# Kernel optimization log

Hardware: AMD Instinct MI355X
Metric: run time of the kernel (lower is better)

## Reference

```python
import jax, jax.numpy as jnp
import numpy as np

TOP_K = 2
LN_EPS = 1e-5
GATE_EPS = 1e-6


def setup_inputs() -> dict:
    key = jax.random.key(0)
    ks = jax.random.split(key, 5)
    B, D, E, H, O = 16384, 1200, 8, 1024, 1
    x = jax.random.normal(ks[0], (B, D), dtype=jnp.float32)
    w_gate = jax.random.normal(ks[1], (D, E), dtype=jnp.float32) * 0.05
    W1 = jax.random.normal(ks[2], (E, D, H), dtype=jnp.float32) * (1.0 / np.sqrt(D))
    b1 = jnp.zeros((E, H), dtype=jnp.float32)
    g1 = jnp.ones((E, H), dtype=jnp.float32)   # LayerNorm weight
    be1 = jnp.zeros((E, H), dtype=jnp.float32)  # LayerNorm bias
    W2 = jax.random.normal(ks[3], (E, H, O), dtype=jnp.float32) * (1.0 / np.sqrt(H))
    b2 = jnp.zeros((E, O), dtype=jnp.float32)
    return {"x": x, "w_gate": w_gate, "W1": W1, "b1": b1, "g1": g1, "be1": be1, "W2": W2, "b2": b2}


def reference(x, w_gate, W1, b1, g1, be1, W2, b2):
    B = x.shape[0]
    # --- top-k gating (eval mode: no noise) ---
    probs = jax.nn.softmax(x @ w_gate, axis=1)                 # [B, E]
    top_vals, top_idx = jax.lax.top_k(probs, TOP_K)            # [B, k]
    top_gates = top_vals / (jnp.sum(top_vals, axis=1, keepdims=True) + GATE_EPS)
    gates = jnp.zeros_like(probs).at[jnp.arange(B)[:, None], top_idx].set(top_gates)  # [B, E]
    # --- per-expert MLP (computed densely for all experts; gates zero out non-selected) ---
    h = jnp.einsum('bd,edh->beh', x, W1) + b1                  # [B, E, H]
    mu = jnp.mean(h, axis=-1, keepdims=True)
    var = jnp.var(h, axis=-1, keepdims=True)
    h = (h - mu) * jax.lax.rsqrt(var + LN_EPS) * g1 + be1      # LayerNorm
    h = jax.nn.relu(h)
    out = jax.nn.sigmoid(jnp.einsum('beh,eho->beo', h, W2) + b2)  # [B, E, O]
    # --- scatter/combine: weighted sum over experts ---
    y = jnp.einsum('be,beo->bo', gates, out)                   # [B, O]
    return y
```

## Files before the change

kernel.cpp:

```cpp
#include <hip/hip_runtime.h>
#include <hip/hip_bf16.h>
#include <stdint.h>

#define B_ROWS 16384
#define D_IN   1200
#define D_PAD  1216
#define N_EXP  8
#define H_DIM  1024
#define CAP    33792
#define N_TILES 264
#define LN_EPS 1e-5f
#define GATE_EPS 1e-6f
#define CNT_STRIDE 16

#define O_CNT    0
#define O_POFF   512
#define O_CNT2   576
#define O_TOPI   1088
#define O_TOPG   132160
#define O_PROWC  263232
#define O_PGATEC 398400
#define O_XBF    533568
#define O_W1T    40381888
#define O_HBUF   60304832

#define GATING_BLOCKS (B_ROWS / 32)
#define W1T_BLOCKS    (19 * 16 * 8)

typedef short bf16x8 __attribute__((ext_vector_type(8)));
typedef short short8 __attribute__((ext_vector_type(8)));
typedef short short4v __attribute__((ext_vector_type(4)));
typedef float f32x4 __attribute__((ext_vector_type(4)));

__device__ __forceinline__ void load_lds16(const void* gptr, void* ldsptr) {
    __builtin_amdgcn_global_load_lds(
        (__attribute__((address_space(1))) void*)const_cast<void*>(gptr),
        (__attribute__((address_space(3))) void*)ldsptr, 16, 0, 0);
}

__device__ __forceinline__ short4v pack_bf16x4(float4 a) {
    union { short4v v; __hip_bfloat16 h[4]; } u;
    u.h[0] = __float2bfloat16(a.x); u.h[1] = __float2bfloat16(a.y);
    u.h[2] = __float2bfloat16(a.z); u.h[3] = __float2bfloat16(a.w);
    return u.v;
}

__global__ __launch_bounds__(256) void gating_w1t_kernel(
    const float* __restrict__ x, const float* __restrict__ wg,
    const float* __restrict__ W1,
    int* __restrict__ topIdx, float* __restrict__ topGate,
    __hip_bfloat16* __restrict__ w1t, __hip_bfloat16* __restrict__ xbf)
{
    __shared__ float tile[2][32][33];
    int bx = blockIdx.x;
    int tid = threadIdx.x;

    if (bx < GATING_BLOCKS) {
        int widx = tid >> 6;
        int lane = tid & 63;
        int rowbase = bx * 32 + widx * 8;
        const float* xw = x + (long)rowbase * D_IN;

        float acc[8][8];
#pragma unroll
        for (int r = 0; r < 8; ++r)
#pragma unroll
            for (int e = 0; e < N_EXP; ++e) acc[r][e] = 0.f;

        for (int i = lane; i < 304; i += 64) {
            if (i < 300) {
                const float4* wv4 = (const float4*)(wg + (long)i * 32);
                float4 w0 = wv4[0], w1v = wv4[1], w2 = wv4[2], w3 = wv4[3],
                       w4 = wv4[4], w5 = wv4[5], w6 = wv4[6], w7 = wv4[7];
#pragma unroll
                for (int r = 0; r < 8; ++r) {
                    float4 xv = ((const float4*)(xw + (long)r * D_IN))[i];
                    acc[r][0] += xv.x * w0.x + xv.y * w2.x + xv.z * w4.x + xv.w * w6.x;
                    acc[r][1] += xv.x * w0.y + xv.y * w2.y + xv.z * w4.y + xv.w * w6.y;
                    acc[r][2] += xv.x * w0.z + xv.y * w2.z + xv.z * w4.z + xv.w * w6.z;
                    acc[r][3] += xv.x * w0.w + xv.y * w2.w + xv.z * w4.w + xv.w * w6.w;
                    acc[r][4] += xv.x * w1v.x + xv.y * w3.x + xv.z * w5.x + xv.w * w7.x;
                    acc[r][5] += xv.x * w1v.y + xv.y * w3.y + xv.z * w5.y + xv.w * w7.y;
                    acc[r][6] += xv.x * w1v.z + xv.y * w3.z + xv.z * w5.z + xv.w * w7.z;
                    acc[r][7] += xv.x * w1v.w + xv.y * w3.w + xv.z * w5.w + xv.w * w7.w;
                    ((short4v*)(xbf + (long)(rowbase + r) * D_PAD))[i] = pack_bf16x4(xv);
                }
            } else {
#pragma unroll
                for (int r = 0; r < 8; ++r)
                    ((short4v*)(xbf + (long)(rowbase + r) * D_PAD))[i] = (short4v){0, 0, 0, 0};
            }
        }

#pragma unroll
        for (int r = 0; r < 8; ++r)
#pragma unroll
            for (int e = 0; e < N_EXP; ++e) {
                float v = acc[r][e];
#pragma unroll
                for (int off = 32; off > 0; off >>= 1) v += __shfl_xor(v, off, 64);
                acc[r][e] = v;
            }

        float my[N_EXP];
#pragma unroll
        for (int e = 0; e < N_EXP; ++e) my[e] = acc[0][e];
#pragma unroll
        for (int r = 1; r < 8; ++r)
#pragma unroll
            for (int e = 0; e < N_EXP; ++e)
                if (lane == r) my[e] = acc[r][e];

        if (lane < 8) {
            float m = my[0];
#pragma unroll
            for (int e = 1; e < N_EXP; ++e) m = fmaxf(m, my[e]);
            float p[N_EXP], s = 0.f;
#pragma unroll
            for (int e = 0; e < N_EXP; ++e) { p[e] = expf(my[e] - m); s += p[e]; }
            int i0 = 0;
#pragma unroll
            for (int e = 1; e < N_EXP; ++e) if (p[e] > p[i0]) i0 = e;
            int i1 = (i0 == 0) ? 1 : 0;
#pragma unroll
            for (int e = 0; e < N_EXP; ++e) if (e != i0 && p[e] > p[i1]) i1 = e;
            float v0 = p[i0] / s, v1 = p[i1] / s;
            float inv = 1.f / (v0 + v1 + GATE_EPS);
            int row = rowbase + lane;
            ((int2*)topIdx)[row] = make_int2(i0, i1);
            ((float2*)topGate)[row] = make_float2(v0 * inv, v1 * inv);
        }
    } else if (bx == GATING_BLOCKS) {
        short8* xrow = (short8*)(xbf + (long)B_ROWS * D_PAD);
        if (tid < 152) xrow[tid] = (short8){0, 0, 0, 0, 0, 0, 0, 0};
    } else {
        int b = bx - GATING_BLOCKS - 1;
        int d0 = (b % 19) * 64;
        int h0 = ((b / 19) % 16) * 64;
        int e = b / (19 * 16);
        const float* src = W1 + (long)e * D_IN * H_DIM;

        int hseg = tid & 7;
        int hs = tid & 15;
        int dr = tid >> 4;
        (void)hseg;
#pragma unroll
        for (int s = 0; s < 4; ++s) {
            int dl = dr + 16 * s;
            int d = d0 + dl;
            float4 v = (d < D_IN)
                ? ((const float4*)(src + (long)d * H_DIM + h0))[hs]
                : (float4){0.f, 0.f, 0.f, 0.f};
            int T = dl >> 5, drl = dl & 31;
            int hl = hs * 4;
            int Th = hl >> 5;
            int hh = hl & 31;
            (void)T; (void)hh;
            tile[Th][drl][hh + 0] = v.x;
            tile[Th][drl][hh + 1] = v.y;
            tile[Th][drl][hh + 2] = v.z;
            tile[Th][drl][hh + 3] = v.w;
            if (s == 1) {
                __syncthreads();
                int r2 = tid;
                int T2 = r2 >> 7, rr = r2 & 127;
                int hl2 = rr >> 2, dseg = rr & 3;
                float f[8];
#pragma unroll
                for (int j = 0; j < 8; ++j) f[j] = tile[T2][dseg * 8 + j][hl2];
                union { short8 v8; __hip_bfloat16 hh8[8]; } u;
#pragma unroll
                for (int j = 0; j < 8; ++j) u.hh8[j] = __float2bfloat16(f[j]);
                int h = h0 + T2 * 32 + hl2;
                ((short8*)(w1t + (long)e * H_DIM * D_PAD + (long)h * D_PAD + d0))[dseg] = u.v8;
                __syncthreads();
            }
        }
        __syncthreads();
        {
            int T2 = tid >> 7, rr = tid & 127;
            int hl2 = rr >> 2, dseg = rr & 3;
            float f[8];
#pragma unroll
            for (int j = 0; j < 8; ++j) f[j] = tile[T2][dseg * 8 + j][hl2];
            union { short8 v8; __hip_bfloat16 hh8[8]; } u;
#pragma unroll
            for (int j = 0; j < 8; ++j) u.hh8[j] = __float2bfloat16(f[j]);
            int h = h0 + T2 * 32 + hl2;
            ((short8*)(w1t + (long)e * H_DIM * D_PAD + (long)h * D_PAD + d0 + 32))[dseg] = u.v8;
        }
    }
}

__global__ __launch_bounds__(256) void hist_kernel(
    const int* __restrict__ topIdx, int* __restrict__ cnt, float* __restrict__ y)
{
    __shared__ int lcnt[N_EXP];
    int tid = threadIdx.x;
    if (tid < N_EXP) lcnt[tid] = 0;
    __syncthreads();
    int row = blockIdx.x * 256 + tid;
    y[row] = 0.f;
    int2 e = ((const int2*)topIdx)[row];
    atomicAdd(&lcnt[e.x], 1);
    atomicAdd(&lcnt[e.y], 1);
    __syncthreads();
    if (tid < N_EXP) atomicAdd(&cnt[tid * CNT_STRIDE], lcnt[tid]);
}

__global__ void offsets_kernel(const int* __restrict__ cnt, int* __restrict__ poff)
{
    if (threadIdx.x == 0 && blockIdx.x == 0) {
        int o = 0;
        for (int e = 0; e < N_EXP; ++e) {
            poff[e] = o;
            o += (cnt[e * CNT_STRIDE] + 127) & ~127;
        }
        poff[N_EXP] = o;
    }
}

__global__ __launch_bounds__(256) void scatter_kernel(
    const int* __restrict__ topIdx, const float* __restrict__ topGate,
    const int* __restrict__ cnt, const int* __restrict__ poff, int* __restrict__ cnt2,
    int* __restrict__ pairRowC, float* __restrict__ pairGateC)
{
    int tid = threadIdx.x;
    int b = blockIdx.x;

    {
        int p = b * 256 + tid;
        int e = 0;
        while (e < N_EXP - 1 && p >= poff[e + 1]) ++e;
        if (p - poff[e] >= cnt[e * CNT_STRIDE]) {
            pairRowC[p] = B_ROWS;
            pairGateC[p] = 0.f;
        }
    }
    if (b >= B_ROWS / 256) return;

    __shared__ int lcnt[N_EXP];
    __shared__ int base[N_EXP];
    if (tid < N_EXP) lcnt[tid] = 0;
    __syncthreads();
    int row = b * 256 + tid;
    int2 e = ((const int2*)topIdx)[row];
    float2 g = ((const float2*)topGate)[row];
    int s0 = atomicAdd(&lcnt[e.x], 1);
    int s1 = atomicAdd(&lcnt[e.y], 1);
    __syncthreads();
    if (tid < N_EXP) base[tid] = atomicAdd(&cnt2[tid * CNT_STRIDE], lcnt[tid]);
    __syncthreads();
    int p0 = poff[e.x] + base[e.x] + s0;
    pairRowC[p0] = row; pairGateC[p0] = g.x;
    int p1 = poff[e.y] + base[e.y] + s1;
    pairRowC[p1] = row; pairGateC[p1] = g.y;
}

__global__ __launch_bounds__(256) void gemm_kernel(
    const __hip_bfloat16* __restrict__ xbf, const __hip_bfloat16* __restrict__ w1t,
    const float* __restrict__ b1, const int* __restrict__ poff,
    const int* __restrict__ pairRowC,
    __hip_bfloat16* __restrict__ hbuf)
{
    int bi = blockIdx.x;
    int xcd = bi & 7;
    int j = bi >> 3;
    int col0 = (j & 7) << 7;
    int rt = xcd * 33 + (j >> 3);
    int row0 = rt << 7;
    if (row0 >= poff[N_EXP]) return;
    int e = 0;
    while (e < N_EXP - 1 && row0 >= poff[e + 1]) ++e;

    __shared__ short lA[128 * 32];
    __shared__ short lB[128 * 32];

    int t = threadIdx.x;
    int lane = t & 63, w = t >> 6;
    int wm = (w >> 1) * 64, wn = (w & 1) * 64;
    int l15 = lane & 15, quad = lane >> 4;
    int qsw = quad ^ ((l15 >> 1) & 3);

    f32x4 acc[4][4];
#pragma unroll
    for (int i = 0; i < 4; ++i)
#pragma unroll
        for (int j2 = 0; j2 < 4; ++j2) acc[i][j2] = (f32x4){0.f, 0.f, 0.f, 0.f};

    int r1 = t >> 2, seg = t & 3;
    int sw = seg ^ ((r1 >> 1) & 3);
    int ridx1 = pairRowC[row0 + r1];
    int ridx2 = pairRowC[row0 + 64 + r1];
    const __hip_bfloat16* Arow1 = xbf + (long)ridx1 * D_PAD + sw * 8;
    const __hip_bfloat16* Arow2 = xbf + (long)ridx2 * D_PAD + sw * 8;
    const __hip_bfloat16* Bb = w1t + (long)e * H_DIM * D_PAD + (long)col0 * D_PAD;
    const __hip_bfloat16* Brow1 = Bb + (long)r1 * D_PAD + sw * 8;
    const __hip_bfloat16* Brow2 = Bb + (long)(r1 + 64) * D_PAD + sw * 8;
    char* lAc = (char*)lA;
    char* lBc = (char*)lB;

    for (int kt = 0; kt < D_PAD / 32; ++kt) {
        __syncthreads();
        int k0 = kt * 32;
        load_lds16(Arow1 + k0, lAc + t * 16);
        load_lds16(Arow2 + k0, lAc + t * 16 + 4096);
        load_lds16(Brow1 + k0, lBc + t * 16);
        load_lds16(Brow2 + k0, lBc + t * 16 + 4096);
        __syncthreads();

        bf16x8 af[4], bfr[4];
#pragma unroll
        for (int i = 0; i < 4; ++i)
            af[i] = *(const bf16x8*)(lAc + (wm + i * 16 + l15) * 64 + qsw * 16);
#pragma unroll
        for (int j2 = 0; j2 < 4; ++j2)
            bfr[j2] = *(const bf16x8*)(lBc + (wn + j2 * 16 + l15) * 64 + qsw * 16);
#pragma unroll
        for (int i = 0; i < 4; ++i)
#pragma unroll
            for (int j2 = 0; j2 < 4; ++j2)
                acc[i][j2] = __builtin_amdgcn_mfma_f32_16x16x32_bf16(af[i], bfr[j2], acc[i][j2], 0, 0, 0);
    }

#pragma unroll
    for (int i = 0; i < 4; ++i) {
        int lr = wm + i * 16 + quad * 4;
#pragma unroll
        for (int j2 = 0; j2 < 4; ++j2) {
            int gc = col0 + wn + j2 * 16 + l15;
            float bias = b1[e * H_DIM + gc];
#pragma unroll
            for (int r = 0; r < 4; ++r) {
                float v = acc[i][j2][r] + bias;
                hbuf[(long)(row0 + lr + r) * H_DIM + gc] = __float2bfloat16(v);
            }
        }
    }
}

__global__ __launch_bounds__(256) void ln_head_kernel(
    const __hip_bfloat16* __restrict__ hbuf, const int* __restrict__ cnt, const int* __restrict__ poff,
    const int* __restrict__ pairRowC, const float* __restrict__ pairGateC,
    const float* __restrict__ g1, const float* __restrict__ be1,
    const float* __restrict__ W2, const float* __restrict__ b2,
    float* __restrict__ y)
{
    int p = blockIdx.x;
    if (p >= poff[N_EXP]) return;
    int e = 0;
    while (e < N_EXP - 1 && p >= poff[e + 1]) ++e;
    if (p - poff[e] >= cnt[e * CNT_STRIDE]) return;

    int row = pairRowC[p];
    float gate = pairGateC[p];
    int tid = threadIdx.x;
    int w = tid >> 6;
    const __hip_bfloat16* hr = hbuf + (long)p * H_DIM;

    union { short4v s; __hip_bfloat16 h[4]; } hv;
    hv.s = ((const short4v*)hr)[tid];
    float v[4];
    float sum = 0.f, sumsq = 0.f;
#pragma unroll
    for (int k = 0; k < 4; ++k) {
        v[k] = __bfloat162float(hv.h[k]);
        sum += v[k];
        sumsq += v[k] * v[k];
    }
#pragma unroll
    for (int off = 32; off > 0; off >>= 1) {
        sum += __shfl_down(sum, off);
        sumsq += __shfl_down(sumsq, off);
    }
    __shared__ float rs[4], rq[4];
    if ((tid & 63) == 0) { rs[w] = sum; rq[w] = sumsq; }
    __syncthreads();
    float tot = rs[0] + rs[1] + rs[2] + rs[3];
    float totq = rq[0] + rq[1] + rq[2] + rq[3];
    float mu = tot * (1.f / H_DIM);
    float var = totq * (1.f / H_DIM) - mu * mu;
    float rstd = rsqrtf(var + LN_EPS);

    float4 gv = ((const float4*)(g1 + e * H_DIM))[tid];
    float4 bv = ((const float4*)(be1 + e * H_DIM))[tid];
    float4 wv = ((const float4*)(W2 + e * H_DIM))[tid];
    float z;
    {
        float hn0 = fmaxf((v[0] - mu) * rstd * gv.x + bv.x, 0.f);
        float hn1 = fmaxf((v[1] - mu) * rstd * gv.y + bv.y, 0.f);
        float hn2 = fmaxf((v[2] - mu) * rstd * gv.z + bv.z, 0.f);
        float hn3 = fmaxf((v[3] - mu) * rstd * gv.w + bv.w, 0.f);
        z = hn0 * wv.x + hn1 * wv.y + hn2 * wv.z + hn3 * wv.w;
    }
#pragma unroll
    for (int off = 32; off > 0; off >>= 1) z += __shfl_down(z, off);
    __syncthreads();
    if ((tid & 63) == 0) rs[w] = z;
    __syncthreads();
    if (tid == 0) {
        float zt = rs[0] + rs[1] + rs[2] + rs[3] + b2[e];
        float o = 1.f / (1.f + expf(-zt));
        atomicAdd(&y[row], gate * o);
    }
}

extern "C" void kernel_launch(void* const* d_in, const int* in_sizes, int n_in,
                              void* d_out, int out_size, void* d_ws, size_t ws_size,
                              hipStream_t stream)
{
    const float* x   = (const float*)d_in[0];
    const float* wg  = (const float*)d_in[1];
    const float* W1  = (const float*)d_in[2];
    const float* b1  = (const float*)d_in[3];
    const float* g1  = (const float*)d_in[4];
    const float* be1 = (const float*)d_in[5];
    const float* W2  = (const float*)d_in[6];
    const float* b2  = (const float*)d_in[7];
    float* y = (float*)d_out;

    char* ws = (char*)d_ws;
    int*   cnt       = (int*)(ws + O_CNT);
    int*   poff      = (int*)(ws + O_POFF);
    int*   cnt2      = (int*)(ws + O_CNT2);
    int*   topIdx    = (int*)(ws + O_TOPI);
    float* topGate   = (float*)(ws + O_TOPG);
    int*   pairRowC  = (int*)(ws + O_PROWC);
    float* pairGateC = (float*)(ws + O_PGATEC);
    __hip_bfloat16* xbf  = (__hip_bfloat16*)(ws + O_XBF);
    __hip_bfloat16* w1t  = (__hip_bfloat16*)(ws + O_W1T);
    __hip_bfloat16* hbuf = (__hip_bfloat16*)(ws + O_HBUF);

    hipMemsetAsync(ws, 0, 1088, stream);

    gating_w1t_kernel<<<GATING_BLOCKS + 1 + W1T_BLOCKS, 256, 0, stream>>>(
        x, wg, W1, topIdx, topGate, w1t, xbf);
    hist_kernel<<<B_ROWS / 256, 256, 0, stream>>>(topIdx, cnt, y);
    offsets_kernel<<<1, 64, 0, stream>>>(cnt, poff);
    scatter_kernel<<<CAP / 256, 256, 0, stream>>>(topIdx, topGate, cnt, poff, cnt2,
                                                  pairRowC, pairGateC);
    gemm_kernel<<<N_TILES * 8, 256, 0, stream>>>(xbf, w1t, b1, poff, pairRowC, hbuf);
    ln_head_kernel<<<CAP, 256, 0, stream>>>(hbuf, cnt, poff, pairRowC, pairGateC,
                                            g1, be1, W2, b2, y);
}
```

Measured before the change: 312.8 us.

## Fuse histogram into gating, deepen GEMM K-step, one wave per row in LN head

Expert counting moves into the gating blocks through an LDS histogram, which removes a separate kernel launch; the zeroing of y moves into the scatter kernel. The GEMM main loop now stages two 32-wide K slices per iteration, halving the number of barrier pairs at the cost of doubled LDS usage. The LayerNorm/head kernel assigns one wavefront per pair row, with four rows per block, so reductions use only shuffles and no block barriers. It also launches a quarter as many blocks.

New measurement: 315.3 us. About the same (+0.8%).

```diff
diff --git a/kernel.cpp b/kernel.cpp
--- a/kernel.cpp
+++ b/kernel.cpp
@@ -49,13 +49,18 @@
     const float* __restrict__ x, const float* __restrict__ wg,
     const float* __restrict__ W1,
     int* __restrict__ topIdx, float* __restrict__ topGate,
+    int* __restrict__ cnt,
     __hip_bfloat16* __restrict__ w1t, __hip_bfloat16* __restrict__ xbf)
 {
     __shared__ float tile[2][32][33];
+    __shared__ int lhist[N_EXP];
     int bx = blockIdx.x;
     int tid = threadIdx.x;
 
     if (bx < GATING_BLOCKS) {
+        if (tid < N_EXP) lhist[tid] = 0;
+        __syncthreads();
+
         int widx = tid >> 6;
         int lane = tid & 63;
         int rowbase = bx * 32 + widx * 8;
@@ -129,7 +134,11 @@
             int row = rowbase + lane;
             ((int2*)topIdx)[row] = make_int2(i0, i1);
             ((float2*)topGate)[row] = make_float2(v0 * inv, v1 * inv);
-        }
+            atomicAdd(&lhist[i0], 1);
+            atomicAdd(&lhist[i1], 1);
+        }
+        __syncthreads();
+        if (tid < N_EXP) atomicAdd(&cnt[tid * CNT_STRIDE], lhist[tid]);
     } else if (bx == GATING_BLOCKS) {
         short8* xrow = (short8*)(xbf + (long)B_ROWS * D_PAD);
         if (tid < 152) xrow[tid] = (short8){0, 0, 0, 0, 0, 0, 0, 0};
@@ -140,10 +149,8 @@
         int e = b / (19 * 16);
         const float* src = W1 + (long)e * D_IN * H_DIM;
 
-        int hseg = tid & 7;
         int hs = tid & 15;
         int dr = tid >> 4;
-        (void)hseg;
 #pragma unroll
         for (int s = 0; s < 4; ++s) {
             int dl = dr + 16 * s;
@@ -151,19 +158,17 @@
             float4 v = (d < D_IN)
                 ? ((const float4*)(src + (long)d * H_DIM + h0))[hs]
                 : (float4){0.f, 0.f, 0.f, 0.f};
-            int T = dl >> 5, drl = dl & 31;
+            int drl = dl & 31;
             int hl = hs * 4;
             int Th = hl >> 5;
             int hh = hl & 31;
-            (void)T; (void)hh;
             tile[Th][drl][hh + 0] = v.x;
             tile[Th][drl][hh + 1] = v.y;
             tile[Th][drl][hh + 2] = v.z;
             tile[Th][drl][hh + 3] = v.w;
             if (s == 1) {
                 __syncthreads();
-                int r2 = tid;
-                int T2 = r2 >> 7, rr = r2 & 127;
+                int T2 = tid >> 7, rr = tid & 127;
                 int hl2 = rr >> 2, dseg = rr & 3;
                 float f[8];
 #pragma unroll
@@ -192,22 +197,6 @@
     }
 }
 
-__global__ __launch_bounds__(256) void hist_kernel(
-    const int* __restrict__ topIdx, int* __restrict__ cnt, float* __restrict__ y)
-{
-    __shared__ int lcnt[N_EXP];
-    int tid = threadIdx.x;
-    if (tid < N_EXP) lcnt[tid] = 0;
-    __syncthreads();
-    int row = blockIdx.x * 256 + tid;
-    y[row] = 0.f;
-    int2 e = ((const int2*)topIdx)[row];
-    atomicAdd(&lcnt[e.x], 1);
-    atomicAdd(&lcnt[e.y], 1);
-    __syncthreads();
-    if (tid < N_EXP) atomicAdd(&cnt[tid * CNT_STRIDE], lcnt[tid]);
-}
-
 __global__ void offsets_kernel(const int* __restrict__ cnt, int* __restrict__ poff)
 {
     if (threadIdx.x == 0 && blockIdx.x == 0) {
@@ -223,7 +212,7 @@
 __global__ __launch_bounds__(256) void scatter_kernel(
     const int* __restrict__ topIdx, const float* __restrict__ topGate,
     const int* __restrict__ cnt, const int* __restrict__ poff, int* __restrict__ cnt2,
-    int* __restrict__ pairRowC, float* __restrict__ pairGateC)
+    int* __restrict__ pairRowC, float* __restrict__ pairGateC, float* __restrict__ y)
 {
     int tid = threadIdx.x;
     int b = blockIdx.x;
@@ -239,11 +228,13 @@
     }
     if (b >= B_ROWS / 256) return;
 
+    int row = b * 256 + tid;
+    y[row] = 0.f;
+
     __shared__ int lcnt[N_EXP];
     __shared__ int base[N_EXP];
     if (tid < N_EXP) lcnt[tid] = 0;
     __syncthreads();
-    int row = b * 256 + tid;
     int2 e = ((const int2*)topIdx)[row];
     float2 g = ((const float2*)topGate)[row];
     int s0 = atomicAdd(&lcnt[e.x], 1);
@@ -273,8 +264,8 @@
     int e = 0;
     while (e < N_EXP - 1 && row0 >= poff[e + 1]) ++e;
 
-    __shared__ short lA[128 * 32];
-    __shared__ short lB[128 * 32];
+    __shared__ short lA[2][128 * 32];
+    __shared__ short lB[2][128 * 32];
 
     int t = threadIdx.x;
     int lane = t & 63, w = t >> 6;
@@ -297,30 +288,37 @@
     const __hip_bfloat16* Bb = w1t + (long)e * H_DIM * D_PAD + (long)col0 * D_PAD;
     const __hip_bfloat16* Brow1 = Bb + (long)r1 * D_PAD + sw * 8;
     const __hip_bfloat16* Brow2 = Bb + (long)(r1 + 64) * D_PAD + sw * 8;
-    char* lAc = (char*)lA;
-    char* lBc = (char*)lB;
-
-    for (int kt = 0; kt < D_PAD / 32; ++kt) {
+
+    for (int kt = 0; kt < D_PAD / 64; ++kt) {
         __syncthreads();
-        int k0 = kt * 32;
-        load_lds16(Arow1 + k0, lAc + t * 16);
-        load_lds16(Arow2 + k0, lAc + t * 16 + 4096);
-        load_lds16(Brow1 + k0, lBc + t * 16);
-        load_lds16(Brow2 + k0, lBc + t * 16 + 4096);
+        int k0 = kt * 64;
+        load_lds16(Arow1 + k0,      (char*)lA[0] + t * 16);
+        load_lds16(Arow2 + k0,      (char*)lA[0] + t * 16 + 4096);
+        load_lds16(Arow1 + k0 + 32, (char*)lA[1] + t * 16);
+        load_lds16(Arow2 + k0 + 32, (char*)lA[1] + t * 16 + 4096);
+        load_lds16(Brow1 + k0,      (char*)lB[0] + t * 16);
+        load_lds16(Brow2 + k0,      (char*)lB[0] + t * 16 + 4096);
+        load_lds16(Brow1 + k0 + 32, (char*)lB[1] + t * 16);
+        load_lds16(Brow2 + k0 + 32, (char*)lB[1] + t * 16 + 4096);
         __syncthreads();
 
-        bf16x8 af[4], bfr[4];
-#pragma unroll
-        for (int i = 0; i < 4; ++i)
-            af[i] = *(const bf16x8*)(lAc + (wm + i * 16 + l15) * 64 + qsw * 16);
-#pragma unroll
-        for (int j2 = 0; j2 < 4; ++j2)
-            bfr[j2] = *(const bf16x8*)(lBc + (wn + j2 * 16 + l15) * 64 + qsw * 16);
-#pragma unroll
-        for (int i = 0; i < 4; ++i)
+#pragma unroll
+        for (int p = 0; p < 2; ++p) {
+            const char* lAc = (const char*)lA[p];
+            const char* lBc = (const char*)lB[p];
+            bf16x8 af[4], bfr[4];
+#pragma unroll
+            for (int i = 0; i < 4; ++i)
+                af[i] = *(const bf16x8*)(lAc + (wm + i * 16 + l15) * 64 + qsw * 16);
 #pragma unroll
             for (int j2 = 0; j2 < 4; ++j2)
-                acc[i][j2] = __builtin_amdgcn_mfma_f32_16x16x32_bf16(af[i], bfr[j2], acc[i][j2], 0, 0, 0);
+                bfr[j2] = *(const bf16x8*)(lBc + (wn + j2 * 16 + l15) * 64 + qsw * 16);
+#pragma unroll
+            for (int i = 0; i < 4; ++i)
+#pragma unroll
+                for (int j2 = 0; j2 < 4; ++j2)
+                    acc[i][j2] = __builtin_amdgcn_mfma_f32_16x16x32_bf16(af[i], bfr[j2], acc[i][j2], 0, 0, 0);
+        }
     }
 
 #pragma unroll
@@ -346,60 +344,56 @@
     const float* __restrict__ W2, const float* __restrict__ b2,
     float* __restrict__ y)
 {
-    int p = blockIdx.x;
+    int tid = threadIdx.x;
+    int p = blockIdx.x * 4 + (tid >> 6);
     if (p >= poff[N_EXP]) return;
     int e = 0;
     while (e < N_EXP - 1 && p >= poff[e + 1]) ++e;
     if (p - poff[e] >= cnt[e * CNT_STRIDE]) return;
 
+    int lane = tid & 63;
     int row = pairRowC[p];
     float gate = pairGateC[p];
-    int tid = threadIdx.x;
-    int w = tid >> 6;
-    const __hip_bfloat16* hr = hbuf + (long)p * H_DIM;
-
-    union { short4v s; __hip_bfloat16 h[4]; } hv;
-    hv.s = ((const short4v*)hr)[tid];
-    float v[4];
+    const short4v* hr = (const short4v*)(hbuf + (long)p * H_DIM);
+
+    float v[16];
     float sum = 0.f, sumsq = 0.f;
 #pragma unroll
     for (int k = 0; k < 4; ++k) {
-        v[k] = __bfloat162float(hv.h[k]);
-        sum += v[k];
-        sumsq += v[k] * v[k];
+        union { short4v s; __hip_bfloat16 h[4]; } hv;
+        hv.s = hr[lane + k * 64];
+#pragma unroll
+        for (int j = 0; j < 4; ++j) {
+            float f = __bfloat162float(hv.h[j]);
+            v[k * 4 + j] = f;
+            sum += f;
+            sumsq += f * f;
+        }
     }
 #pragma unroll
     for (int off = 32; off > 0; off >>= 1) {
-        sum += __shfl_down(sum, off);
-        sumsq += __shfl_down(sumsq, off);
-    }
-    __shared__ float rs[4], rq[4];
-    if ((tid & 63) == 0) { rs[w] = sum; rq[w] = sumsq; }
-    __syncthreads();
-    float tot = rs[0] + rs[1] + rs[2] + rs[3];
-    float totq = rq[0] + rq[1] + rq[2] + rq[3];
-    float mu = tot * (1.f / H_DIM);
-    float var = totq * (1.f / H_DIM) - mu * mu;
+        sum += __shfl_xor(sum, off, 64);
+        sumsq += __shfl_xor(sumsq, off, 64);
+    }
+    float mu = sum * (1.f / H_DIM);
+    float var = sumsq * (1.f / H_DIM) - mu * mu;
     float rstd = rsqrtf(var + LN_EPS);
 
-    float4 gv = ((const float4*)(g1 + e * H_DIM))[tid];
-    float4 bv = ((const float4*)(be1 + e * H_DIM))[tid];
-    float4 wv = ((const float4*)(W2 + e * H_DIM))[tid];
-    float z;
-    {
-        float hn0 = fmaxf((v[0] - mu) * rstd * gv.x + bv.x, 0.f);
-        float hn1 = fmaxf((v[1] - mu) * rstd * gv.y + bv.y, 0.f);
-        float hn2 = fmaxf((v[2] - mu) * rstd * gv.z + bv.z, 0.f);
-        float hn3 = fmaxf((v[3] - mu) * rstd * gv.w + bv.w, 0.f);
-        z = hn0 * wv.x + hn1 * wv.y + hn2 * wv.z + hn3 * wv.w;
-    }
-#pragma unroll
-    for (int off = 32; off > 0; off >>= 1) z += __shfl_down(z, off);
-    __syncthreads();
-    if ((tid & 63) == 0) rs[w] = z;
-    __syncthreads();
-    if (tid == 0) {
-        float zt = rs[0] + rs[1] + rs[2] + rs[3] + b2[e];
+    float z = 0.f;
+#pragma unroll
+    for (int k = 0; k < 4; ++k) {
+        float4 gv = ((const float4*)(g1 + e * H_DIM))[lane + k * 64];
+        float4 bv = ((const float4*)(be1 + e * H_DIM))[lane + k * 64];
+        float4 wv = ((const float4*)(W2 + e * H_DIM))[lane + k * 64];
+        z += fmaxf((v[k*4+0] - mu) * rstd * gv.x + bv.x, 0.f) * wv.x;
+        z += fmaxf((v[k*4+1] - mu) * rstd * gv.y + bv.y, 0.f) * wv.y;
+        z += fmaxf((v[k*4+2] - mu) * rstd * gv.z + bv.z, 0.f) * wv.z;
+        z += fmaxf((v[k*4+3] - mu) * rstd * gv.w + bv.w, 0.f) * wv.w;
+    }
+#pragma unroll
+    for (int off = 32; off > 0; off >>= 1) z += __shfl_xor(z, off, 64);
+    if (lane == 0) {
+        float zt = z + b2[e];
         float o = 1.f / (1.f + expf(-zt));
         atomicAdd(&y[row], gate * o);
     }
@@ -434,12 +428,11 @@
     hipMemsetAsync(ws, 0, 1088, stream);
 
     gating_w1t_kernel<<<GATING_BLOCKS + 1 + W1T_BLOCKS, 256, 0, stream>>>(
-        x, wg, W1, topIdx, topGate, w1t, xbf);
-    hist_kernel<<<B_ROWS / 256, 256, 0, stream>>>(topIdx, cnt, y);
+        x, wg, W1, topIdx, topGate, cnt, w1t, xbf);
     offsets_kernel<<<1, 64, 0, stream>>>(cnt, poff);
     scatter_kernel<<<CAP / 256, 256, 0, stream>>>(topIdx, topGate, cnt, poff, cnt2,
-                                                  pairRowC, pairGateC);
+                                                  pairRowC, pairGateC, y);
     gemm_kernel<<<N_TILES * 8, 256, 0, stream>>>(xbf, w1t, b1, poff, pairRowC, hbuf);
-    ln_head_kernel<<<CAP, 256, 0, stream>>>(hbuf, cnt, poff, pairRowC, pairGateC,
-                                            g1, be1, W2, b2, y);
-}
+    ln_head_kernel<<<(CAP + 3) / 4, 256, 0, stream>>>(hbuf, cnt, poff, pairRowC, pairGateC,
+                                                      g1, be1, W2, b2, y);
+}
```
